# Kernel optimization log

Hardware: AMD Instinct MI355X
Metric: run time of the kernel (lower is better)

The kernel has to match this reference:

```python
import jax, jax.numpy as jnp
import numpy as np

MIN_SEGMENT_PIXELS = 50
NUM_SEG_IDS = 32  # segment ids in [0, 32); 0 = background


def setup_inputs() -> dict:
    key = jax.random.key(0)
    k1, k2 = jax.random.split(key)
    B, H, W = 16, 512, 1024
    flow = jax.random.normal(k1, (B, 2, H, W), dtype=jnp.float32)
    masks = jax.random.randint(k2, (B, H, W), 0, NUM_SEG_IDS, dtype=jnp.int32)
    return {"flow": flow, "masks": masks}


def reference(flow, masks):
    B, _, H, W = flow.shape
    S = NUM_SEG_IDS
    # Global segment id = b * S + seg_id so one fused segment_sum covers all batches.
    gid = (masks.reshape(B, -1) + jnp.arange(B, dtype=masks.dtype)[:, None] * S).reshape(-1)
    u = flow[:, 0].reshape(-1)
    v = flow[:, 1].reshape(-1)
    nseg = B * S
    cnt = jax.ops.segment_sum(jnp.ones_like(u), gid, num_segments=nseg)
    su  = jax.ops.segment_sum(u,     gid, num_segments=nseg)
    suu = jax.ops.segment_sum(u * u, gid, num_segments=nseg)
    sv  = jax.ops.segment_sum(v,     gid, num_segments=nseg)
    svv = jax.ops.segment_sum(v * v, gid, num_segments=nseg)
    safe_cnt = jnp.maximum(cnt, 1.0)
    denom = jnp.maximum(cnt - 1.0, 1.0)  # torch .var() is unbiased (ddof=1)
    var_u = (suu - su * su / safe_cnt) / denom
    var_v = (svv - sv * sv / safe_cnt) / denom
    is_bg = (jnp.arange(nseg) % S) == 0  # seg_id == 0 skipped
    valid = (cnt >= MIN_SEGMENT_PIXELS) & (~is_bg)
    total = jnp.sum(jnp.where(valid, var_u + var_v, 0.0))
    n = jnp.sum(valid.astype(flow.dtype))
    return jnp.where(n > 0, total / jnp.maximum(n, 1.0), 0.0)
```

## Files before the change

kernel.cpp:

```cpp
#include <hip/hip_runtime.h>

#define BATCH 16
#define NSEG 32
#define HW (512 * 1024)
#define MIN_PIX 50.0f

#define THREADS 64
#define CHUNKS 64
#define PIX_PER_BLOCK (HW / CHUNKS)
#define VEC 4
#define ITERS (PIX_PER_BLOCK / (THREADS * VEC))

#define ACC_FLOATS (BATCH * NSEG * 4)

__global__ __launch_bounds__(THREADS) void ovl_accum(
    const float* __restrict__ flow,
    const int* __restrict__ masks,
    float* __restrict__ acc)
{
    __shared__ float4 bins[THREADS][NSEG];

    const int tid = threadIdx.x;
    #pragma unroll
    for (int i = 0; i < NSEG; ++i)
        bins[tid][i] = make_float4(0.0f, 0.0f, 0.0f, 0.0f);
    __syncthreads();

    const int b = blockIdx.y;
    const int chunk = blockIdx.x;
    const float* __restrict__ u_base = flow + (size_t)b * 2 * HW;
    const float* __restrict__ v_base = u_base + HW;
    const int*   __restrict__ m_base = masks + (size_t)b * HW;
    const int p0 = chunk * PIX_PER_BLOCK;

#define LOADP(S, IT) { const int p = p0 + ((IT) * THREADS + tid) * VEC;        \
        m##S = *(const int4*)(m_base + p);                                    \
        u##S = *(const float4*)(u_base + p);                                  \
        v##S = *(const float4*)(v_base + p); }

#define PROC1(mm, uu, vv) { const int s = (mm) & (NSEG - 1);                   \
        float4 cur = bins[tid][s];                                            \
        cur.x += 1.0f; cur.y += (uu); cur.z += (vv);                          \
        cur.w += (uu) * (uu) + (vv) * (vv);                                   \
        bins[tid][s] = cur; }

#define PROCP(S) { PROC1(m##S.x, u##S.x, v##S.x) PROC1(m##S.y, u##S.y, v##S.y) \
        PROC1(m##S.z, u##S.z, v##S.z) PROC1(m##S.w, u##S.w, v##S.w) }

    int4 mA, mB; float4 uA, vA, uB, vB;
    LOADP(A, 0)
    LOADP(B, 1)
    #pragma unroll
    for (int it = 0; it < ITERS; it += 2) {
        PROCP(A)
        if (it + 2 < ITERS) LOADP(A, it + 2)
        PROCP(B)
        if (it + 3 < ITERS) LOADP(B, it + 3)
    }
    __syncthreads();

    const float* smf = (const float*)bins;
    #pragma unroll
    for (int pair = tid; pair < NSEG * 4; pair += THREADS) {
        float sum = 0.0f;
        #pragma unroll
        for (int j = 0; j < THREADS; ++j)
            sum += smf[j * NSEG * 4 + pair];
        unsafeAtomicAdd(&acc[(size_t)b * NSEG * 4 + pair], sum);
    }
}

__global__ __launch_bounds__(BATCH * NSEG) void ovl_finalize(
    const float* __restrict__ acc,
    float* __restrict__ out)
{
    const int tid = threadIdx.x;
    const float cnt = acc[tid * 4 + 0];
    const float su  = acc[tid * 4 + 1];
    const float sv  = acc[tid * 4 + 2];
    const float s2  = acc[tid * 4 + 3];

    const bool is_bg = (tid & (NSEG - 1)) == 0;
    const bool valid = (cnt >= MIN_PIX) && !is_bg;

    const float safe_cnt = fmaxf(cnt, 1.0f);
    const float denom = fmaxf(cnt - 1.0f, 1.0f);
    const float var_sum = (s2 - (su * su + sv * sv) / safe_cnt) / denom;

    float t = valid ? var_sum : 0.0f;
    float n = valid ? 1.0f : 0.0f;

    #pragma unroll
    for (int off = 32; off >= 1; off >>= 1) {
        t += __shfl_down(t, off, 64);
        n += __shfl_down(n, off, 64);
    }

    __shared__ float st[8], sn[8];
    const int wave = tid >> 6;
    const int lane = tid & 63;
    if (lane == 0) { st[wave] = t; sn[wave] = n; }
    __syncthreads();

    if (tid == 0) {
        float tot = 0.0f, ntot = 0.0f;
        #pragma unroll
        for (int w = 0; w < 8; ++w) { tot += st[w]; ntot += sn[w]; }
        out[0] = (ntot > 0.0f) ? (tot / fmaxf(ntot, 1.0f)) : 0.0f;
    }
}

extern "C" void kernel_launch(void* const* d_in, const int* in_sizes, int n_in,
                              void* d_out, int out_size, void* d_ws, size_t ws_size,
                              hipStream_t stream) {
    const float* flow = (const float*)d_in[0];
    const int* masks  = (const int*)d_in[1];
    float* out = (float*)d_out;
    float* acc = (float*)d_ws;

    hipMemsetAsync(acc, 0, ACC_FLOATS * sizeof(float), stream);

    dim3 grid(CHUNKS, BATCH);
    ovl_accum<<<grid, THREADS, 0, stream>>>(flow, masks, acc);
    ovl_finalize<<<1, BATCH * NSEG, 0, stream>>>(acc, out);
}
```

Measured before the change: 31.10 us.

## Split bin components across lane pairs with shuffle exchange and halve LDS bins

Each lane pair now shares the work for a pixel pair. Lanes swap segment ids and flow values with xor shuffles, and each lane keeps only two of the four statistics (count/u or v/sumsq) in a float2 bin row. A spare bin slot absorbs the merged update when both pixels hit the same segment. This halves shared memory per block, which should raise occupancy. The grid also doubles to 128 blocks per batch with an interleaved global access pattern. The cost is extra shuffles and selects per pixel, plus two LDS read-modify-writes per round instead of one.

```diff
diff --git a/kernel.cpp b/kernel.cpp
--- a/kernel.cpp
+++ b/kernel.cpp
@@ -6,10 +6,10 @@
 #define MIN_PIX 50.0f
 
 #define THREADS 64
-#define CHUNKS 64
-#define PIX_PER_BLOCK (HW / CHUNKS)
+#define BLOCKS_PER_BATCH 128
+#define ITERS 16
 #define VEC 4
-#define ITERS (PIX_PER_BLOCK / (THREADS * VEC))
+#define ROWW 34
 
 #define ACC_FLOATS (BATCH * NSEG * 4)
 
@@ -18,55 +18,72 @@
     const int* __restrict__ masks,
     float* __restrict__ acc)
 {
-    __shared__ float4 bins[THREADS][NSEG];
+    __shared__ float2 bins[THREADS][ROWW];
 
     const int tid = threadIdx.x;
     #pragma unroll
-    for (int i = 0; i < NSEG; ++i)
-        bins[tid][i] = make_float4(0.0f, 0.0f, 0.0f, 0.0f);
-    __syncthreads();
+    for (int j = 0; j < ROWW; ++j)
+        bins[tid][j] = make_float2(0.0f, 0.0f);
 
-    const int b = blockIdx.y;
-    const int chunk = blockIdx.x;
+    const int b  = blockIdx.x >> 7;
+    const int bk = blockIdx.x & (BLOCKS_PER_BATCH - 1);
     const float* __restrict__ u_base = flow + (size_t)b * 2 * HW;
     const float* __restrict__ v_base = u_base + HW;
     const int*   __restrict__ m_base = masks + (size_t)b * HW;
-    const int p0 = chunk * PIX_PER_BLOCK;
+    const int par = tid & 1;
 
-#define LOADP(S, IT) { const int p = p0 + ((IT) * THREADS + tid) * VEC;        \
-        m##S = *(const int4*)(m_base + p);                                    \
-        u##S = *(const float4*)(u_base + p);                                  \
+#define LOADP(S, IT) { const int p = ((IT) * BLOCKS_PER_BATCH + bk) * (THREADS * VEC) + tid * VEC; \
+        m##S = *(const int4*)(m_base + p);                                                         \
+        u##S = *(const float4*)(u_base + p);                                                       \
         v##S = *(const float4*)(v_base + p); }
 
-#define PROC1(mm, uu, vv) { const int s = (mm) & (NSEG - 1);                   \
-        float4 cur = bins[tid][s];                                            \
-        cur.x += 1.0f; cur.y += (uu); cur.z += (vv);                          \
-        cur.w += (uu) * (uu) + (vv) * (vv);                                   \
-        bins[tid][s] = cur; }
+#define ROUND(ss, uu, vv) {                                                    \
+        const int   s  = (ss) & (NSEG - 1);                                    \
+        const float u  = (uu), v = (vv);                                       \
+        const int   sp = __shfl_xor(s, 1, 64);                                 \
+        const float up = __shfl_xor(u, 1, 64);                                 \
+        const float vp = __shfl_xor(v, 1, 64);                                 \
+        float2 dS, dP;                                                         \
+        dS.x = par ? v  : 1.0f;  dS.y = par ? (u * u + v * v)    : u;          \
+        dP.x = par ? vp : 1.0f;  dP.y = par ? (up * up + vp * vp) : up;        \
+        const bool dup = (s == sp);                                            \
+        if (dup) { dS.x += dP.x; dS.y += dP.y; }                               \
+        const int spe = dup ? 32 : sp;                                         \
+        float2 x0 = bins[tid][s];                                              \
+        float2 x1 = bins[tid][spe];                                            \
+        x0.x += dS.x; x0.y += dS.y;                                            \
+        x1.x += dP.x; x1.y += dP.y;                                            \
+        bins[tid][s]   = x0;                                                   \
+        bins[tid][spe] = x1;                                                   \
+    }
 
-#define PROCP(S) { PROC1(m##S.x, u##S.x, v##S.x) PROC1(m##S.y, u##S.y, v##S.y) \
-        PROC1(m##S.z, u##S.z, v##S.z) PROC1(m##S.w, u##S.w, v##S.w) }
+#define PROCQ(S) { ROUND(m##S.x, u##S.x, v##S.x) ROUND(m##S.y, u##S.y, v##S.y) \
+                   ROUND(m##S.z, u##S.z, v##S.z) ROUND(m##S.w, u##S.w, v##S.w) }
 
     int4 mA, mB; float4 uA, vA, uB, vB;
     LOADP(A, 0)
     LOADP(B, 1)
-    #pragma unroll
     for (int it = 0; it < ITERS; it += 2) {
-        PROCP(A)
+        PROCQ(A)
         if (it + 2 < ITERS) LOADP(A, it + 2)
-        PROCP(B)
+        PROCQ(B)
         if (it + 3 < ITERS) LOADP(B, it + 3)
     }
+
     __syncthreads();
 
-    const float* smf = (const float*)bins;
+    const float* bf = (const float*)bins;
     #pragma unroll
-    for (int pair = tid; pair < NSEG * 4; pair += THREADS) {
+    for (int h = 0; h < 2; ++h) {
+        const int p = tid + h * 64;
+        const int s = p >> 2, c = p & 3;
+        const int parr = c >> 1;
+        const int comp = c & 1;
         float sum = 0.0f;
         #pragma unroll
-        for (int j = 0; j < THREADS; ++j)
-            sum += smf[j * NSEG * 4 + pair];
-        unsafeAtomicAdd(&acc[(size_t)b * NSEG * 4 + pair], sum);
+        for (int j = 0; j < 32; ++j)
+            sum += bf[((2 * j + parr) * ROWW + s) * 2 + comp];
+        unsafeAtomicAdd(&acc[((size_t)b * NSEG + s) * 4 + c], sum);
     }
 }
 
@@ -120,7 +137,6 @@
 
     hipMemsetAsync(acc, 0, ACC_FLOATS * sizeof(float), stream);
 
-    dim3 grid(CHUNKS, BATCH);
-    ovl_accum<<<grid, THREADS, 0, stream>>>(flow, masks, acc);
+    ovl_accum<<<BATCH * BLOCKS_PER_BATCH, THREADS, 0, stream>>>(flow, masks, acc);
     ovl_finalize<<<1, BATCH * NSEG, 0, stream>>>(acc, out);
 }
```

Result: slower. 39.48 us (+26.9%).

## Double grid size, interleave block access, merge duplicate bins within each pixel quad

Applied to the files above, without the earlier changes.

Doubles the number of blocks per batch (128 instead of 64) in a flat 1D grid. Each block now strides through the image with interleaved quads instead of reading one contiguous chunk. Within each group of 4 pixels, contributions that share a segment id are merged in registers, then applied with four independent LDS read-modify-writes. This breaks the serial read-after-write chain through shared memory. The post-zeroing barrier is dropped, which is safe only because each thread touches just its own bin row. The cost is more ALU work for the comparisons and selects.

```diff
diff --git a/kernel.cpp b/kernel.cpp
--- a/kernel.cpp
+++ b/kernel.cpp
@@ -6,10 +6,8 @@
 #define MIN_PIX 50.0f
 
 #define THREADS 64
-#define CHUNKS 64
-#define PIX_PER_BLOCK (HW / CHUNKS)
-#define VEC 4
-#define ITERS (PIX_PER_BLOCK / (THREADS * VEC))
+#define BLOCKS_PER_BATCH 128
+#define QUADS 16
 
 #define ACC_FLOATS (BATCH * NSEG * 4)
 
@@ -24,48 +22,78 @@
     #pragma unroll
     for (int i = 0; i < NSEG; ++i)
         bins[tid][i] = make_float4(0.0f, 0.0f, 0.0f, 0.0f);
-    __syncthreads();
 
-    const int b = blockIdx.y;
-    const int chunk = blockIdx.x;
+    const int b  = blockIdx.x >> 7;
+    const int bk = blockIdx.x & (BLOCKS_PER_BATCH - 1);
     const float* __restrict__ u_base = flow + (size_t)b * 2 * HW;
     const float* __restrict__ v_base = u_base + HW;
     const int*   __restrict__ m_base = masks + (size_t)b * HW;
-    const int p0 = chunk * PIX_PER_BLOCK;
 
-#define LOADP(S, IT) { const int p = p0 + ((IT) * THREADS + tid) * VEC;        \
-        m##S = *(const int4*)(m_base + p);                                    \
-        u##S = *(const float4*)(u_base + p);                                  \
+#define LOADP(S, Q) { const int p = (((Q) * BLOCKS_PER_BATCH + bk) * THREADS + tid) * 4; \
+        m##S = *(const int4*)(m_base + p);                                               \
+        u##S = *(const float4*)(u_base + p);                                             \
         v##S = *(const float4*)(v_base + p); }
 
-#define PROC1(mm, uu, vv) { const int s = (mm) & (NSEG - 1);                   \
-        float4 cur = bins[tid][s];                                            \
-        cur.x += 1.0f; cur.y += (uu); cur.z += (vv);                          \
-        cur.w += (uu) * (uu) + (vv) * (vv);                                   \
-        bins[tid][s] = cur; }
-
-#define PROCP(S) { PROC1(m##S.x, u##S.x, v##S.x) PROC1(m##S.y, u##S.y, v##S.y) \
-        PROC1(m##S.z, u##S.z, v##S.z) PROC1(m##S.w, u##S.w, v##S.w) }
+#define PROCQ(mq, uq, vq) {                                                    \
+        const int s0 = mq.x & 31, s1 = mq.y & 31, s2 = mq.z & 31, s3 = mq.w & 31; \
+        float d0c = 1.0f, d0u = uq.x, d0v = vq.x, d0w = uq.x*uq.x + vq.x*vq.x; \
+        float d1c = 1.0f, d1u = uq.y, d1v = vq.y, d1w = uq.y*uq.y + vq.y*vq.y; \
+        float d2c = 1.0f, d2u = uq.z, d2v = vq.z, d2w = uq.z*uq.z + vq.z*vq.z; \
+        float d3c = 1.0f, d3u = uq.w, d3v = vq.w, d3w = uq.w*uq.w + vq.w*vq.w; \
+        const bool m10 = (s1 == s0);                                           \
+        const bool m20 = (s2 == s0), m21 = !m20 && (s2 == s1);                 \
+        const bool m30 = (s3 == s0), m31 = !m30 && (s3 == s1);                 \
+        const bool m32 = !m30 && !m31 && (s3 == s2);                           \
+        d0c += m10 ? d1c : 0.0f; d0u += m10 ? d1u : 0.0f;                      \
+        d0v += m10 ? d1v : 0.0f; d0w += m10 ? d1w : 0.0f;                      \
+        d0c += m20 ? d2c : 0.0f; d0u += m20 ? d2u : 0.0f;                      \
+        d0v += m20 ? d2v : 0.0f; d0w += m20 ? d2w : 0.0f;                      \
+        d1c += m21 ? d2c : 0.0f; d1u += m21 ? d2u : 0.0f;                      \
+        d1v += m21 ? d2v : 0.0f; d1w += m21 ? d2w : 0.0f;                      \
+        d0c += m30 ? d3c : 0.0f; d0u += m30 ? d3u : 0.0f;                      \
+        d0v += m30 ? d3v : 0.0f; d0w += m30 ? d3w : 0.0f;                      \
+        d1c += m31 ? d3c : 0.0f; d1u += m31 ? d3u : 0.0f;                      \
+        d1v += m31 ? d3v : 0.0f; d1w += m31 ? d3w : 0.0f;                      \
+        d2c += m32 ? d3c : 0.0f; d2u += m32 ? d3u : 0.0f;                      \
+        d2v += m32 ? d3v : 0.0f; d2w += m32 ? d3w : 0.0f;                      \
+        const float k1 = m10 ? 0.0f : 1.0f;                                    \
+        const float k2 = (m20 || m21) ? 0.0f : 1.0f;                           \
+        const float k3 = (m30 || m31 || m32) ? 0.0f : 1.0f;                    \
+        float4 x0 = bins[tid][s0];                                             \
+        float4 x1 = bins[tid][s1];                                             \
+        float4 x2 = bins[tid][s2];                                             \
+        float4 x3 = bins[tid][s3];                                             \
+        x0.x += d0c;      x0.y += d0u;      x0.z += d0v;      x0.w += d0w;     \
+        x1.x += k1 * d1c; x1.y += k1 * d1u; x1.z += k1 * d1v; x1.w += k1 * d1w;\
+        x2.x += k2 * d2c; x2.y += k2 * d2u; x2.z += k2 * d2v; x2.w += k2 * d2w;\
+        x3.x += k3 * d3c; x3.y += k3 * d3u; x3.z += k3 * d3v; x3.w += k3 * d3w;\
+        bins[tid][s3] = x3;                                                    \
+        bins[tid][s2] = x2;                                                    \
+        bins[tid][s1] = x1;                                                    \
+        bins[tid][s0] = x0;                                                    \
+    }
 
     int4 mA, mB; float4 uA, vA, uB, vB;
     LOADP(A, 0)
     LOADP(B, 1)
     #pragma unroll
-    for (int it = 0; it < ITERS; it += 2) {
-        PROCP(A)
-        if (it + 2 < ITERS) LOADP(A, it + 2)
-        PROCP(B)
-        if (it + 3 < ITERS) LOADP(B, it + 3)
+    for (int q = 0; q < QUADS; q += 2) {
+        PROCQ(mA, uA, vA)
+        if (q + 2 < QUADS) LOADP(A, q + 2)
+        PROCQ(mB, uB, vB)
+        if (q + 3 < QUADS) LOADP(B, q + 3)
     }
+
     __syncthreads();
 
-    const float* smf = (const float*)bins;
+    const float* bf = (const float*)bins;
     #pragma unroll
-    for (int pair = tid; pair < NSEG * 4; pair += THREADS) {
+    for (int h = 0; h < 2; ++h) {
+        const int pair = tid + h * 64;
         float sum = 0.0f;
         #pragma unroll
         for (int j = 0; j < THREADS; ++j)
-            sum += smf[j * NSEG * 4 + pair];
+            sum += bf[j * (NSEG * 4) + pair];
         unsafeAtomicAdd(&acc[(size_t)b * NSEG * 4 + pair], sum);
     }
 }
@@ -120,7 +148,6 @@
 
     hipMemsetAsync(acc, 0, ACC_FLOATS * sizeof(float), stream);
 
-    dim3 grid(CHUNKS, BATCH);
-    ovl_accum<<<grid, THREADS, 0, stream>>>(flow, masks, acc);
+    ovl_accum<<<BATCH * BLOCKS_PER_BATCH, THREADS, 0, stream>>>(flow, masks, acc);
     ovl_finalize<<<1, BATCH * NSEG, 0, stream>>>(acc, out);
 }
```

After: 44.82 us. 1.44x slower.

## Replace per-thread LDS histogram with register one-hot accumulation using packed FMA

Applied to the files above, without the earlier changes.

Each thread now keeps all 32 segment bins in registers and updates every bin per pixel with a one-hot mask multiply using packed two-wide float math, removing the dependent LDS read-modify-write chains of the old shared-memory histogram. The grid becomes 128 blocks per batch with pixels interleaved across blocks, and the final reduction runs in four LDS passes through a padded buffer with a shuffle and atomics. The cost is 32x more ALU work per pixel and a high register count (launch bounds request 2 blocks).

```diff
diff --git a/kernel.cpp b/kernel.cpp
--- a/kernel.cpp
+++ b/kernel.cpp
@@ -6,68 +6,88 @@
 #define MIN_PIX 50.0f
 
 #define THREADS 64
-#define CHUNKS 64
-#define PIX_PER_BLOCK (HW / CHUNKS)
-#define VEC 4
-#define ITERS (PIX_PER_BLOCK / (THREADS * VEC))
+#define BPB 128
+#define QUADS 16
 
 #define ACC_FLOATS (BATCH * NSEG * 4)
 
-__global__ __launch_bounds__(THREADS) void ovl_accum(
+typedef float f32x2 __attribute__((ext_vector_type(2)));
+
+__global__ __launch_bounds__(THREADS, 2) void ovl_accum(
     const float* __restrict__ flow,
     const int* __restrict__ masks,
     float* __restrict__ acc)
 {
-    __shared__ float4 bins[THREADS][NSEG];
+    __shared__ float red[THREADS][NSEG + 1];
 
     const int tid = threadIdx.x;
-    #pragma unroll
-    for (int i = 0; i < NSEG; ++i)
-        bins[tid][i] = make_float4(0.0f, 0.0f, 0.0f, 0.0f);
-    __syncthreads();
-
-    const int b = blockIdx.y;
-    const int chunk = blockIdx.x;
+    const int b  = blockIdx.x >> 7;
+    const int bk = blockIdx.x & (BPB - 1);
     const float* __restrict__ u_base = flow + (size_t)b * 2 * HW;
     const float* __restrict__ v_base = u_base + HW;
     const int*   __restrict__ m_base = masks + (size_t)b * HW;
-    const int p0 = chunk * PIX_PER_BLOCK;
 
-#define LOADP(S, IT) { const int p = p0 + ((IT) * THREADS + tid) * VEC;        \
-        m##S = *(const int4*)(m_base + p);                                    \
-        u##S = *(const float4*)(u_base + p);                                  \
+    f32x2 acc_uv[NSEG];
+    f32x2 acc_c2[NSEG];
+    #pragma unroll
+    for (int s = 0; s < NSEG; ++s) {
+        acc_uv[s] = (f32x2)(0.0f);
+        acc_c2[s] = (f32x2)(0.0f);
+    }
+
+#define LOADP(S, Q) { const int p = (((Q) * BPB + bk) * THREADS + tid) * 4; \
+        m##S = *(const int4*)(m_base + p);                                  \
+        u##S = *(const float4*)(u_base + p);                                \
         v##S = *(const float4*)(v_base + p); }
 
-#define PROC1(mm, uu, vv) { const int s = (mm) & (NSEG - 1);                   \
-        float4 cur = bins[tid][s];                                            \
-        cur.x += 1.0f; cur.y += (uu); cur.z += (vv);                          \
-        cur.w += (uu) * (uu) + (vv) * (vv);                                   \
-        bins[tid][s] = cur; }
+#define PX(mm, uu, vv) {                                                    \
+        const float u_ = (uu), v_ = (vv);                                   \
+        const int   m_ = (mm) & (NSEG - 1);                                 \
+        const float s2_ = fmaf(u_, u_, v_ * v_);                            \
+        const f32x2 uv_ = {u_, v_};                                         \
+        const f32x2 c2_ = {1.0f, s2_};                                      \
+        _Pragma("unroll")                                                   \
+        for (int s = 0; s < NSEG; ++s) {                                    \
+            const float k = (m_ == s) ? 1.0f : 0.0f;                        \
+            const f32x2 k2 = {k, k};                                        \
+            acc_uv[s] += k2 * uv_;                                          \
+            acc_c2[s] += k2 * c2_;                                          \
+        }                                                                   \
+    }
 
-#define PROCP(S) { PROC1(m##S.x, u##S.x, v##S.x) PROC1(m##S.y, u##S.y, v##S.y) \
-        PROC1(m##S.z, u##S.z, v##S.z) PROC1(m##S.w, u##S.w, v##S.w) }
+#define PROCQ(mq, uq, vq) { PX(mq.x, uq.x, vq.x) PX(mq.y, uq.y, vq.y)       \
+                            PX(mq.z, uq.z, vq.z) PX(mq.w, uq.w, vq.w) }
 
     int4 mA, mB; float4 uA, vA, uB, vB;
     LOADP(A, 0)
     LOADP(B, 1)
-    #pragma unroll
-    for (int it = 0; it < ITERS; it += 2) {
-        PROCP(A)
-        if (it + 2 < ITERS) LOADP(A, it + 2)
-        PROCP(B)
-        if (it + 3 < ITERS) LOADP(B, it + 3)
+    #pragma unroll 1
+    for (int q = 0; q < QUADS; q += 2) {
+        PROCQ(mA, uA, vA)
+        if (q + 2 < QUADS) LOADP(A, q + 2)
+        PROCQ(mB, uB, vB)
+        if (q + 3 < QUADS) LOADP(B, q + 3)
     }
-    __syncthreads();
 
-    const float* smf = (const float*)bins;
-    #pragma unroll
-    for (int pair = tid; pair < NSEG * 4; pair += THREADS) {
-        float sum = 0.0f;
-        #pragma unroll
-        for (int j = 0; j < THREADS; ++j)
-            sum += smf[j * NSEG * 4 + pair];
-        unsafeAtomicAdd(&acc[(size_t)b * NSEG * 4 + pair], sum);
+#define RPASS(EXPR, CIDX) {                                                 \
+        _Pragma("unroll")                                                   \
+        for (int s = 0; s < NSEG; ++s) red[tid][s] = (EXPR);                \
+        __syncthreads();                                                    \
+        const int rs = tid >> 1, rh = tid & 1;                              \
+        float sum = 0.0f;                                                   \
+        _Pragma("unroll")                                                   \
+        for (int i = 0; i < 32; ++i)                                        \
+            sum += red[rh * 32 + ((i + tid) & 31)][rs];                     \
+        sum += __shfl_xor(sum, 1, 64);                                      \
+        if (rh == 0)                                                        \
+            unsafeAtomicAdd(&acc[((size_t)b * NSEG + rs) * 4 + (CIDX)], sum);\
+        __syncthreads();                                                    \
     }
+
+    RPASS(acc_c2[s].x, 0)
+    RPASS(acc_uv[s].x, 1)
+    RPASS(acc_uv[s].y, 2)
+    RPASS(acc_c2[s].y, 3)
 }
 
 __global__ __launch_bounds__(BATCH * NSEG) void ovl_finalize(
@@ -120,7 +140,6 @@
 
     hipMemsetAsync(acc, 0, ACC_FLOATS * sizeof(float), stream);
 
-    dim3 grid(CHUNKS, BATCH);
-    ovl_accum<<<grid, THREADS, 0, stream>>>(flow, masks, acc);
+    ovl_accum<<<BATCH * BPB, THREADS, 0, stream>>>(flow, masks, acc);
     ovl_finalize<<<1, BATCH * NSEG, 0, stream>>>(acc, out);
 }
```

After: 66.17 us. 2.13x slower.
